# Optimization experiments

Measured on AMD Instinct MI355X. Metric: run time of the kernel, lower is better.

The kernel has to match this reference:

```python
import jax, jax.numpy as jnp
import numpy as np

N_WAY = 5
N_SHOT = 10

def setup_inputs() -> dict:
    key = jax.random.key(0)
    k1, k2, k3, k4 = jax.random.split(key, 4)
    B, n_support, n_query, T, F, D = 32, 50, 75, 128, 64, 256
    support_x = jax.random.normal(k1, (B, n_support, T, F), dtype=jnp.float32)
    query_x = jax.random.normal(k2, (B, n_query, T, F), dtype=jnp.float32)
    # episodic labels: every class present exactly N_SHOT times per episode
    support_y = jnp.broadcast_to(jnp.repeat(jnp.arange(N_WAY), N_SHOT)[None, :], (B, n_support))
    W = jax.random.normal(k3, (F, D), dtype=jnp.float32) * 0.05
    b = jax.random.normal(k4, (D,), dtype=jnp.float32) * 0.05
    return {"support_x": support_x, "support_y": support_y, "query_x": query_x, "W": W, "b": b}

def _encode(x, W, b):
    # mean-pool over time, then linear projection: [B, N, T, F] -> [B, N, D]
    return jnp.einsum('bntf,fd->bnd', x, W) / x.shape[2] + b

def reference(support_x, support_y, query_x, W, b):
    B, n_query = query_x.shape[0], query_x.shape[1]
    support_z = _encode(support_x, W, b)   # [B, S, D]
    query_z = _encode(query_x, W, b)       # [B, Q, D]
    # label-grouped mean (prototypes) via one-hot segment sum, all episodes at once
    onehot = (support_y[..., None] == jnp.arange(N_WAY)).astype(support_z.dtype)  # [B, S, K]
    counts = onehot.sum(axis=1)                                                   # [B, K]
    prototypes = jnp.einsum('bsk,bsd->bkd', onehot, support_z) / counts[..., None]
    # Euclidean cdist: [B, Q, K]
    diff = query_z[:, :, None, :] - prototypes[:, None, :, :]
    dists = jnp.sqrt(jnp.sum(diff * diff, axis=-1))
    logits = -dists
    return logits.reshape(B * n_query, N_WAY)
```

## Files before the change

kernel.cpp:

```cpp
#include <hip/hip_runtime.h>
#include <math.h>

#define B_  32
#define NS_ 50
#define NQ_ 75
#define T_  128
#define F_  64
#define D_  256
#define K_  5
#define NR_ (NS_ + NQ_)
#define QT_ 5
#define NTILE_ 15

typedef float v4f __attribute__((ext_vector_type(4)));

__global__ __launch_bounds__(256) void meanpool_kernel(
    const float* __restrict__ sx, const float* __restrict__ qx,
    float* __restrict__ meanbuf)
{
    const int wave = threadIdx.x >> 6, lane = threadIdx.x & 63;
    const int item = blockIdx.x * 4 + wave;
    const int b = item / NR_, n = item % NR_;
    const float* src = (n < NS_)
        ? (sx + (size_t)(b * NS_ + n) * (T_ * F_))
        : (qx + (size_t)(b * NQ_ + (n - NS_)) * (T_ * F_));
    const v4f* src4 = (const v4f*)src;

    v4f a0 = 0.f, a1 = 0.f, a2 = 0.f, a3 = 0.f;
#pragma unroll
    for (int s = 0; s < 32; s += 4) {
        v4f v0 = __builtin_nontemporal_load(&src4[(s + 0) * 64 + lane]);
        v4f v1 = __builtin_nontemporal_load(&src4[(s + 1) * 64 + lane]);
        v4f v2 = __builtin_nontemporal_load(&src4[(s + 2) * 64 + lane]);
        v4f v3 = __builtin_nontemporal_load(&src4[(s + 3) * 64 + lane]);
        a0 += v0; a1 += v1; a2 += v2; a3 += v3;
    }
    v4f a = (a0 + a1) + (a2 + a3);

    a.x += __shfl_down(a.x, 32); a.y += __shfl_down(a.y, 32);
    a.z += __shfl_down(a.z, 32); a.w += __shfl_down(a.w, 32);
    a.x += __shfl_down(a.x, 16); a.y += __shfl_down(a.y, 16);
    a.z += __shfl_down(a.z, 16); a.w += __shfl_down(a.w, 16);

    if (lane < 16)
        ((v4f*)meanbuf)[(size_t)item * 16 + lane] = a * (1.f / T_);
}

__global__ __launch_bounds__(256) void proto_kernel(
    const float* __restrict__ meanbuf, const int* __restrict__ sy,
    const float* __restrict__ Wm, const float* __restrict__ bias,
    float* __restrict__ out)
{
    __shared__ float rows[QT_ + K_][F_];
    __shared__ float zbuf[QT_ + K_][D_];
    __shared__ int   labels[NS_];
    __shared__ float psum[K_][F_];
    __shared__ int   counts[K_];

    const int tid = threadIdx.x;
    const int bid = blockIdx.x;
    const int b = bid / NTILE_, qt = bid % NTILE_;
    const int q0 = qt * QT_;

    if (tid < NS_) labels[tid] = sy[b * NS_ + tid];
    __syncthreads();

    if (tid < F_) {
        const int f = tid;
        float p0 = 0.f, p1 = 0.f, p2 = 0.f, p3 = 0.f, p4 = 0.f;
        for (int s = 0; s < NS_; ++s) {
            float v = meanbuf[((size_t)b * NR_ + s) * F_ + f];
            int l = labels[s];
            if      (l == 0) p0 += v;
            else if (l == 1) p1 += v;
            else if (l == 2) p2 += v;
            else if (l == 3) p3 += v;
            else             p4 += v;
        }
        psum[0][f] = p0; psum[1][f] = p1; psum[2][f] = p2;
        psum[3][f] = p3; psum[4][f] = p4;
    }
    if (tid < K_) {
        int c = 0;
        for (int s = 0; s < NS_; ++s) c += (labels[s] == tid);
        counts[tid] = c;
    }
    for (int i = tid; i < QT_ * F_; i += 256) {
        int r = i / F_, f = i % F_;
        rows[r][f] = meanbuf[((size_t)b * NR_ + NS_ + q0 + r) * F_ + f];
    }
    __syncthreads();
    for (int i = tid; i < K_ * F_; i += 256) {
        int k = i / F_, f = i % F_;
        rows[QT_ + k][f] = psum[k][f] / (float)counts[k];
    }
    __syncthreads();

    {
        const int d = tid;
        float wreg[F_];
#pragma unroll
        for (int f = 0; f < F_; ++f) wreg[f] = Wm[f * D_ + d];
        const float bd = bias[d];
        for (int r = 0; r < QT_ + K_; ++r) {
            const float2* row2 = (const float2*)rows[r];
            float acc = bd;
#pragma unroll
            for (int f2 = 0; f2 < F_ / 2; ++f2) {
                float2 rv = row2[f2];
                acc += rv.x * wreg[2 * f2] + rv.y * wreg[2 * f2 + 1];
            }
            zbuf[r][d] = acc;
        }
    }
    __syncthreads();

    const int wave = tid >> 6, lane = tid & 63;
    for (int p = wave; p < QT_ * K_; p += 4) {
        const int q = p / K_, k = p % K_;
        float s = 0.f;
#pragma unroll
        for (int j = 0; j < 4; ++j) {
            int d = lane + j * 64;
            float diff = zbuf[q][d] - zbuf[QT_ + k][d];
            s += diff * diff;
        }
        for (int off = 32; off > 0; off >>= 1) s += __shfl_down(s, off);
        if (lane == 0) out[(size_t)(b * NQ_ + q0 + q) * K_ + k] = -sqrtf(s);
    }
}

extern "C" void kernel_launch(void* const* d_in, const int* in_sizes, int n_in,
                              void* d_out, int out_size, void* d_ws, size_t ws_size,
                              hipStream_t stream) {
    const float* sx   = (const float*)d_in[0];
    const int*   sy   = (const int*)  d_in[1];
    const float* qx   = (const float*)d_in[2];
    const float* Wm   = (const float*)d_in[3];
    const float* bias = (const float*)d_in[4];
    float* out = (float*)d_out;
    float* meanbuf = (float*)d_ws;

    meanpool_kernel<<<(B_ * NR_) / 4, 256, 0, stream>>>(sx, qx, meanbuf);
    proto_kernel<<<B_ * NTILE_, 256, 0, stream>>>(meanbuf, sy, Wm, bias, out);
}
```

Before: 172.5 us.

## Fuse linear projection into mean-pool kernel and average prototypes in embedding space

The projection by W and bias moves into the mean-pool kernel, so each wave projects its own pooled row and writes the D-dimensional embedding to workspace. The distance kernel then builds prototypes by averaging the support embeddings rather than projecting averaged inputs, and drops its per-block 64-register W load and the redundant re-projection of prototypes in every query tile. In exchange the workspace traffic grows from F to D floats per row, and the first kernel picks up an extra block barrier plus the W reads.

Result: no change. 174.0 us (+0.9%).

```diff
diff --git a/kernel.cpp b/kernel.cpp
--- a/kernel.cpp
+++ b/kernel.cpp
@@ -14,10 +14,13 @@
 
 typedef float v4f __attribute__((ext_vector_type(4)));
 
-__global__ __launch_bounds__(256) void meanpool_kernel(
+__global__ __launch_bounds__(256) void meanproj_kernel(
     const float* __restrict__ sx, const float* __restrict__ qx,
-    float* __restrict__ meanbuf)
+    const float* __restrict__ Wm, const float* __restrict__ bias,
+    float* __restrict__ zbuf)
 {
+    __shared__ float mean_s[4][F_];
+
     const int wave = threadIdx.x >> 6, lane = threadIdx.x & 63;
     const int item = blockIdx.x * 4 + wave;
     const int b = item / NR_, n = item % NR_;
@@ -43,33 +46,53 @@
     a.z += __shfl_down(a.z, 16); a.w += __shfl_down(a.w, 16);
 
     if (lane < 16)
-        ((v4f*)meanbuf)[(size_t)item * 16 + lane] = a * (1.f / T_);
+        ((v4f*)mean_s[wave])[lane] = a * (1.f / T_);
+    __syncthreads();
+
+    const v4f* W4 = (const v4f*)Wm;
+    const float* ms = mean_s[wave];
+    v4f accA = ((const v4f*)bias)[lane];
+    v4f accB = 0.f;
+#pragma unroll
+    for (int f = 0; f < F_; f += 2) {
+        accA += ms[f]     * W4[(f    ) * 64 + lane];
+        accB += ms[f + 1] * W4[(f + 1) * 64 + lane];
+    }
+    ((v4f*)zbuf)[(size_t)item * 64 + lane] = accA + accB;
 }
 
-__global__ __launch_bounds__(256) void proto_kernel(
-    const float* __restrict__ meanbuf, const int* __restrict__ sy,
-    const float* __restrict__ Wm, const float* __restrict__ bias,
+__global__ __launch_bounds__(256) void dist_kernel(
+    const float* __restrict__ zbuf, const int* __restrict__ sy,
     float* __restrict__ out)
 {
-    __shared__ float rows[QT_ + K_][F_];
-    __shared__ float zbuf[QT_ + K_][D_];
+    __shared__ float qz[QT_][D_];
+    __shared__ float pz[K_][D_];
     __shared__ int   labels[NS_];
-    __shared__ float psum[K_][F_];
     __shared__ int   counts[K_];
 
     const int tid = threadIdx.x;
     const int bid = blockIdx.x;
     const int b = bid / NTILE_, qt = bid % NTILE_;
     const int q0 = qt * QT_;
+    const float* zb = zbuf + (size_t)b * NR_ * D_;
 
     if (tid < NS_) labels[tid] = sy[b * NS_ + tid];
+#pragma unroll
+    for (int r = 0; r < QT_; ++r)
+        qz[r][tid] = zb[(NS_ + q0 + r) * D_ + tid];
     __syncthreads();
 
-    if (tid < F_) {
-        const int f = tid;
+    if (tid < K_) {
+        int c = 0;
+        for (int s = 0; s < NS_; ++s) c += (labels[s] == tid);
+        counts[tid] = c;
+    }
+
+    {
+        const int d = tid;
         float p0 = 0.f, p1 = 0.f, p2 = 0.f, p3 = 0.f, p4 = 0.f;
         for (int s = 0; s < NS_; ++s) {
-            float v = meanbuf[((size_t)b * NR_ + s) * F_ + f];
+            float v = zb[s * D_ + d];
             int l = labels[s];
             if      (l == 0) p0 += v;
             else if (l == 1) p1 += v;
@@ -77,41 +100,12 @@
             else if (l == 3) p3 += v;
             else             p4 += v;
         }
-        psum[0][f] = p0; psum[1][f] = p1; psum[2][f] = p2;
-        psum[3][f] = p3; psum[4][f] = p4;
-    }
-    if (tid < K_) {
-        int c = 0;
-        for (int s = 0; s < NS_; ++s) c += (labels[s] == tid);
-        counts[tid] = c;
-    }
-    for (int i = tid; i < QT_ * F_; i += 256) {
-        int r = i / F_, f = i % F_;
-        rows[r][f] = meanbuf[((size_t)b * NR_ + NS_ + q0 + r) * F_ + f];
-    }
-    __syncthreads();
-    for (int i = tid; i < K_ * F_; i += 256) {
-        int k = i / F_, f = i % F_;
-        rows[QT_ + k][f] = psum[k][f] / (float)counts[k];
-    }
-    __syncthreads();
-
-    {
-        const int d = tid;
-        float wreg[F_];
-#pragma unroll
-        for (int f = 0; f < F_; ++f) wreg[f] = Wm[f * D_ + d];
-        const float bd = bias[d];
-        for (int r = 0; r < QT_ + K_; ++r) {
-            const float2* row2 = (const float2*)rows[r];
-            float acc = bd;
-#pragma unroll
-            for (int f2 = 0; f2 < F_ / 2; ++f2) {
-                float2 rv = row2[f2];
-                acc += rv.x * wreg[2 * f2] + rv.y * wreg[2 * f2 + 1];
-            }
-            zbuf[r][d] = acc;
-        }
+        __syncthreads();
+        pz[0][d] = p0 / (float)counts[0];
+        pz[1][d] = p1 / (float)counts[1];
+        pz[2][d] = p2 / (float)counts[2];
+        pz[3][d] = p3 / (float)counts[3];
+        pz[4][d] = p4 / (float)counts[4];
     }
     __syncthreads();
 
@@ -122,7 +116,7 @@
 #pragma unroll
         for (int j = 0; j < 4; ++j) {
             int d = lane + j * 64;
-            float diff = zbuf[q][d] - zbuf[QT_ + k][d];
+            float diff = qz[q][d] - pz[k][d];
             s += diff * diff;
         }
         for (int off = 32; off > 0; off >>= 1) s += __shfl_down(s, off);
@@ -138,9 +132,9 @@
     const float* qx   = (const float*)d_in[2];
     const float* Wm   = (const float*)d_in[3];
     const float* bias = (const float*)d_in[4];
-    float* out = (float*)d_out;
-    float* meanbuf = (float*)d_ws;
+    float* out  = (float*)d_out;
+    float* zbuf = (float*)d_ws;
 
-    meanpool_kernel<<<(B_ * NR_) / 4, 256, 0, stream>>>(sx, qx, meanbuf);
-    proto_kernel<<<B_ * NTILE_, 256, 0, stream>>>(meanbuf, sy, Wm, bias, out);
+    meanproj_kernel<<<(B_ * NR_) / 4, 256, 0, stream>>>(sx, qx, Wm, bias, zbuf);
+    dist_kernel<<<B_ * NTILE_, 256, 0, stream>>>(zbuf, sy, out);
 }
```
